# Kernel optimization log

Measured on AMD Instinct MI355X. Metric: run time of the kernel, lower is better.

The kernel has to match this reference:

```python
import jax, jax.numpy as jnp
import numpy as np

PERTURBATION_SCALE = 0.01

def setup_inputs() -> dict:
    key = jax.random.key(0)
    k1, k2, k3 = jax.random.split(key, 3)
    theta = jax.random.normal(k1, (256, 512), dtype=jnp.float32)
    basis_eval = jax.random.normal(k2, (100000, 512), dtype=jnp.float32)
    noise = jax.random.normal(k3, (256, 512), dtype=jnp.float32)
    return {"theta": theta, "basis_eval": basis_eval, "noise": noise}

def reference(theta, basis_eval, noise):
    # phi: [N, K] functional evaluations
    phi_raw = basis_eval @ theta.T
    phi_perturbed = basis_eval @ (theta + noise * PERTURBATION_SCALE).T
    # sign-crossings between consecutive evaluation points: [N-1, K]
    crossings = (phi_raw[:-1] * phi_raw[1:] < 0).astype(theta.dtype)
    crossings_p = (phi_perturbed[:-1] * phi_perturbed[1:] < 0).astype(theta.dtype)
    persistence = crossings * crossings_p  # [N-1, K]
    # fused pairwise shared-persistence: Gram matrix [K, K]
    gram = persistence.T @ persistence
    K = theta.shape[0]
    iu, ju = jnp.triu_indices(K, k=1)  # row-major i<j == itertools.combinations order
    return gram[iu, ju]  # [K*(K-1)/2]
```

## Files before the change

### kernel.cpp

```cpp
#include <hip/hip_runtime.h>
#include <hip/hip_bf16.h>
#include <stdint.h>

#define KDIM    256
#define NWORDS  1564
#define NW      1563
#define GEMM_GRID 1564

typedef float  f32x4  __attribute__((ext_vector_type(4)));
typedef __bf16 bf16x8 __attribute__((ext_vector_type(8)));

__device__ __forceinline__ void gl_lds16(const void* g, void* l) {
    __builtin_amdgcn_global_load_lds(
        (const __attribute__((address_space(1))) unsigned int*)g,
        (__attribute__((address_space(3))) unsigned int*)l, 16, 0, 0);
}

__global__ void build_w(const float* __restrict__ theta,
                        const float* __restrict__ noise,
                        __bf16* __restrict__ W) {
    int idx = blockIdx.x * 256 + threadIdx.x;
    int j = idx >> 9;
    int d = idx & 511;
    float v;
    if (j < KDIM) v = theta[j * 512 + d];
    else          v = theta[(j - KDIM) * 512 + d] + 0.01f * noise[(j - KDIM) * 512 + d];
    W[idx] = (__bf16)v;
}

__global__ void __launch_bounds__(512, 2)
gemm_signs(const float* __restrict__ basis,
           const __bf16* __restrict__ W,
           uint64_t* __restrict__ sbits) {
    __shared__ char smem[65536];

    const int tid    = threadIdx.x;
    const int lane   = tid & 63;
    const int wave   = tid >> 6;
    const int wr     = wave >> 2;
    const int wc     = wave & 3;
    const int lane16 = lane & 15;
    const int lgrp   = lane >> 4;

    const int orig = blockIdx.x;
    const int xcd  = orig & 7;
    const int wgid = (xcd < 4 ? xcd * 196 : 784 + (xcd - 4) * 195) + (orig >> 3);
    const int bn   = wgid & 1;
    const int bm   = wgid >> 1;

    auto stage = [&](int t) {
        char* abase = smem + ((t & 1) << 14);
        char* bbase = smem + 32768 + ((t & 1) << 14);
        #pragma unroll
        for (int i = 0; i < 2; ++i) {
            int r = wave * 16 + i * 8 + (lane >> 3);
            int g = lane & 7;
            int rg = bm * 128 + r; if (rg > 99999) rg = 99999;
            const float* src = basis + (size_t)rg * 512 + t * 32 + ((g ^ (r & 7)) << 2);
            gl_lds16(src, abase + (wave * 16 + i * 8) * 128);
        }
        #pragma unroll
        for (int i = 0; i < 2; ++i) {
            int c = wave * 32 + i * 16 + (lane >> 2);
            int g = lane & 3;
            const __bf16* src = W + (size_t)(bn * 256 + c) * 512 + t * 32
                                  + ((g ^ ((c >> 1) & 3)) << 3);
            gl_lds16(src, bbase + (wave * 32 + i * 16) * 64);
        }
    };

    stage(0);
    stage(1);

    f32x4 acc[4][4] = {};
    const int s = lane16 & 7;

    #pragma unroll
    for (int t = 0; t < 16; ++t) {
        if (t < 15) asm volatile("s_waitcnt vmcnt(4)\ns_barrier" ::: "memory");
        else        asm volatile("s_waitcnt vmcnt(0)\ns_barrier" ::: "memory");

        const char* ab = smem + ((t & 1) << 14);
        const char* bb = smem + 32768 + ((t & 1) << 14);

        bf16x8 bf[4];
        #pragma unroll
        for (int n = 0; n < 4; ++n) {
            int cc = wc * 64 + n * 16 + lane16;
            int gb = lgrp ^ ((cc >> 1) & 3);
            bf[n] = *(const bf16x8*)(bb + cc * 64 + gb * 16);
        }

        #pragma unroll
        for (int mh = 0; mh < 2; ++mh) {
            bf16x8 af[2];
            #pragma unroll
            for (int mi = 0; mi < 2; ++mi) {
                int rr = wr * 64 + (mh * 2 + mi) * 16 + lane16;
                f32x4 lo = *(const f32x4*)(ab + rr * 128 + (((2 * lgrp + 0) ^ s) << 4));
                f32x4 hi = *(const f32x4*)(ab + rr * 128 + (((2 * lgrp + 1) ^ s) << 4));
                af[mi][0] = (__bf16)lo[0]; af[mi][1] = (__bf16)lo[1];
                af[mi][2] = (__bf16)lo[2]; af[mi][3] = (__bf16)lo[3];
                af[mi][4] = (__bf16)hi[0]; af[mi][5] = (__bf16)hi[1];
                af[mi][6] = (__bf16)hi[2]; af[mi][7] = (__bf16)hi[3];
            }
            __builtin_amdgcn_s_setprio(1);
            #pragma unroll
            for (int mi = 0; mi < 2; ++mi)
                #pragma unroll
                for (int n = 0; n < 4; ++n)
                    acc[mh * 2 + mi][n] = __builtin_amdgcn_mfma_f32_16x16x32_bf16(
                        af[mi], bf[n], acc[mh * 2 + mi][n], 0, 0, 0);
            __builtin_amdgcn_s_setprio(0);
        }

        asm volatile("s_barrier" ::: "memory");
        if (t < 14) stage(t + 2);
    }

    unsigned char* sb = (unsigned char*)smem;
    #pragma unroll
    for (int m = 0; m < 4; ++m) {
        #pragma unroll
        for (int n = 0; n < 4; ++n) {
            int cc = wc * 64 + n * 16 + lane16;
            int rb = wr * 64 + m * 16 + lgrp * 4;
            uint32_t pk = 0;
            #pragma unroll
            for (int r = 0; r < 4; ++r)
                pk |= (acc[m][n][r] < 0.0f ? 1u : 0u) << (8 * r);
            *(uint32_t*)&sb[cc * 136 + rb] = pk;
        }
    }
    asm volatile("s_waitcnt lgkmcnt(0)\ns_barrier" ::: "memory");

    {
        const int col = tid & 255;
        const int wh  = tid >> 8;
        const unsigned char* src = &sb[col * 136 + wh * 64];
        uint64_t wbits = 0;
        #pragma unroll
        for (int k = 0; k < 16; ++k) {
            uint32_t q  = *(const uint32_t*)&src[4 * k];
            uint32_t p4 = ((q & 0x01010101u) * 0x10204080u) >> 28;
            wbits |= (uint64_t)p4 << (4 * k);
        }
        sbits[(size_t)(bm * 2 + wh) * 512 + bn * 256 + col] = wbits;
    }
}

__global__ void crossing_masks(const uint64_t* __restrict__ sbits,
                               uint64_t* __restrict__ maskT) {
    const int w = blockIdx.x;
    const int j = threadIdx.x;
    uint64_t s0r = sbits[(size_t)w * 512 + j];
    uint64_t s0p = sbits[(size_t)w * 512 + 256 + j];
    uint64_t s1r = sbits[(size_t)(w + 1) * 512 + j];
    uint64_t s1p = sbits[(size_t)(w + 1) * 512 + 256 + j];
    uint64_t cr = s0r ^ ((s0r >> 1) | (s1r << 63));
    uint64_t cp = s0p ^ ((s0p >> 1) | (s1p << 63));
    uint64_t m = cr & cp;
    if (w == NW - 1) m &= 0x7FFFFFFFull;
    maskT[(size_t)w * 256 + j] = m;
}

__global__ void zero_out(float* __restrict__ out) {
    int i = blockIdx.x * 256 + threadIdx.x;
    if (i < 32640) out[i] = 0.0f;
}

__global__ void pair_popcount(const uint64_t* __restrict__ maskT,
                              float* __restrict__ out) {
    const int i = blockIdx.x;
    const int c = blockIdx.y;
    const int j = threadIdx.x;
    if (j <= i) return;
    int w0 = c * 391;
    int w1 = w0 + 391; if (w1 > NW) w1 = NW;
    uint32_t sum = 0;
    #pragma unroll 4
    for (int w = w0; w < w1; ++w) {
        uint64_t mi = maskT[(size_t)w * 256 + i];
        uint64_t mj = maskT[(size_t)w * 256 + j];
        sum += (uint32_t)__popcll(mi & mj);
    }
    const size_t idx = (size_t)i * (2 * KDIM - i - 1) / 2 + (size_t)(j - i - 1);
    atomicAdd(&out[idx], (float)sum);
}

extern "C" void kernel_launch(void* const* d_in, const int* in_sizes, int n_in,
                              void* d_out, int out_size, void* d_ws, size_t ws_size,
                              hipStream_t stream) {
    const float* theta = (const float*)d_in[0];
    const float* basis = (const float*)d_in[1];
    const float* noise = (const float*)d_in[2];
    float* out = (float*)d_out;

    char* ws = (char*)d_ws;
    __bf16*   W     = (__bf16*)ws;
    uint64_t* sbits = (uint64_t*)(ws + 524288);
    uint64_t* maskT = (uint64_t*)(ws + 524288 + (size_t)NWORDS * 512 * 8);

    hipLaunchKernelGGL(build_w,        dim3(1024),     dim3(256), 0, stream, theta, noise, W);
    hipLaunchKernelGGL(gemm_signs,     dim3(GEMM_GRID),dim3(512), 0, stream, basis, W, sbits);
    hipLaunchKernelGGL(crossing_masks, dim3(NW),       dim3(256), 0, stream, sbits, maskT);
    hipLaunchKernelGGL(zero_out,       dim3(128),      dim3(256), 0, stream, out);
    hipLaunchKernelGGL(pair_popcount,  dim3(KDIM, 4),  dim3(256), 0, stream, maskT, out);
}
```

Baseline: 125.4 us.

## Stage A tile through registers as bf16 in LDS and raise GEMM occupancy

The GEMM kernel now loads the fp32 basis rows into registers, converts them to bf16 once, and stores them into a half-size LDS buffer. Previously fp32 went straight to LDS and was converted after every fragment read. This shrinks LDS to 48KB so launch bounds can request 4 blocks per SM, and it removes repeated conversion work from the MFMA loop. The A prefetch is register double-buffered with a different waitcnt schedule. Separately, pair_popcount is split into 8 chunks instead of 4 for more parallelism, at the cost of more atomics. Risks are register pressure from 4-block occupancy and extra VMEM latency exposure from the register path.

```diff
diff --git a/kernel.cpp b/kernel.cpp
--- a/kernel.cpp
+++ b/kernel.cpp
@@ -28,11 +28,11 @@
     W[idx] = (__bf16)v;
 }
 
-__global__ void __launch_bounds__(512, 2)
+__global__ void __launch_bounds__(512, 4)
 gemm_signs(const float* __restrict__ basis,
            const __bf16* __restrict__ W,
            uint64_t* __restrict__ sbits) {
-    __shared__ char smem[65536];
+    __shared__ char smem[49152];
 
     const int tid    = threadIdx.x;
     const int lane   = tid & 63;
@@ -48,17 +48,14 @@
     const int bn   = wgid & 1;
     const int bm   = wgid >> 1;
 
-    auto stage = [&](int t) {
-        char* abase = smem + ((t & 1) << 14);
-        char* bbase = smem + 32768 + ((t & 1) << 14);
-        #pragma unroll
-        for (int i = 0; i < 2; ++i) {
-            int r = wave * 16 + i * 8 + (lane >> 3);
-            int g = lane & 7;
-            int rg = bm * 128 + r; if (rg > 99999) rg = 99999;
-            const float* src = basis + (size_t)rg * 512 + t * 32 + ((g ^ (r & 7)) << 2);
-            gl_lds16(src, abase + (wave * 16 + i * 8) * 128);
-        }
+    const int ar = tid >> 2;
+    const int ah = tid & 3;
+    int arg = bm * 128 + ar; if (arg > 99999) arg = 99999;
+    const float* abase_g = basis + (size_t)arg * 512 + ah * 8;
+    const int awofs = ar * 64 + ((ah ^ (ar & 3)) << 4);
+
+    auto stage_B = [&](int t) {
+        char* bbase = smem + 16384 + ((t & 1) << 14);
         #pragma unroll
         for (int i = 0; i < 2; ++i) {
             int c = wave * 32 + i * 16 + (lane >> 2);
@@ -69,19 +66,38 @@
         }
     };
 
-    stage(0);
-    stage(1);
-
-    f32x4 acc[4][4] = {};
-    const int s = lane16 & 7;
+    f32x4  acc[4][4] = {};
+    float4 ra[2][2];
+
+    ra[0][0] = *(const float4*)(abase_g);
+    ra[0][1] = *(const float4*)(abase_g + 4);
+    ra[1][0] = *(const float4*)(abase_g + 32);
+    ra[1][1] = *(const float4*)(abase_g + 36);
+    stage_B(0);
+    asm volatile("s_waitcnt vmcnt(4)" ::: "memory");
+    {
+        bf16x8 a8;
+        a8[0] = (__bf16)ra[0][0].x; a8[1] = (__bf16)ra[0][0].y;
+        a8[2] = (__bf16)ra[0][0].z; a8[3] = (__bf16)ra[0][0].w;
+        a8[4] = (__bf16)ra[0][1].x; a8[5] = (__bf16)ra[0][1].y;
+        a8[6] = (__bf16)ra[0][1].z; a8[7] = (__bf16)ra[0][1].w;
+        *(bf16x8*)(smem + awofs) = a8;
+    }
 
     #pragma unroll
     for (int t = 0; t < 16; ++t) {
-        if (t < 15) asm volatile("s_waitcnt vmcnt(4)\ns_barrier" ::: "memory");
-        else        asm volatile("s_waitcnt vmcnt(0)\ns_barrier" ::: "memory");
-
-        const char* ab = smem + ((t & 1) << 14);
-        const char* bb = smem + 32768 + ((t & 1) << 14);
+        if (t < 14) {
+            ra[t & 1][0] = *(const float4*)(abase_g + (t + 2) * 32);
+            ra[t & 1][1] = *(const float4*)(abase_g + (t + 2) * 32 + 4);
+        }
+        if (t < 15) stage_B(t + 1);
+
+        if      (t < 14) asm volatile("s_waitcnt vmcnt(4)\ns_barrier" ::: "memory");
+        else if (t == 14) asm volatile("s_waitcnt vmcnt(2)\ns_barrier" ::: "memory");
+        else              asm volatile("s_waitcnt vmcnt(0)\ns_barrier" ::: "memory");
+
+        const char* ab = smem + ((t & 1) << 13);
+        const char* bb = smem + 16384 + ((t & 1) << 14);
 
         bf16x8 bf[4];
         #pragma unroll
@@ -90,32 +106,32 @@
             int gb = lgrp ^ ((cc >> 1) & 3);
             bf[n] = *(const bf16x8*)(bb + cc * 64 + gb * 16);
         }
-
-        #pragma unroll
-        for (int mh = 0; mh < 2; ++mh) {
-            bf16x8 af[2];
+        bf16x8 af[4];
+        #pragma unroll
+        for (int m = 0; m < 4; ++m) {
+            int rr = wr * 64 + m * 16 + lane16;
+            af[m] = *(const bf16x8*)(ab + rr * 64 + ((lgrp ^ (rr & 3)) << 4));
+        }
+
+        __builtin_amdgcn_s_setprio(1);
+        #pragma unroll
+        for (int m = 0; m < 4; ++m)
             #pragma unroll
-            for (int mi = 0; mi < 2; ++mi) {
-                int rr = wr * 64 + (mh * 2 + mi) * 16 + lane16;
-                f32x4 lo = *(const f32x4*)(ab + rr * 128 + (((2 * lgrp + 0) ^ s) << 4));
-                f32x4 hi = *(const f32x4*)(ab + rr * 128 + (((2 * lgrp + 1) ^ s) << 4));
-                af[mi][0] = (__bf16)lo[0]; af[mi][1] = (__bf16)lo[1];
-                af[mi][2] = (__bf16)lo[2]; af[mi][3] = (__bf16)lo[3];
-                af[mi][4] = (__bf16)hi[0]; af[mi][5] = (__bf16)hi[1];
-                af[mi][6] = (__bf16)hi[2]; af[mi][7] = (__bf16)hi[3];
-            }
-            __builtin_amdgcn_s_setprio(1);
-            #pragma unroll
-            for (int mi = 0; mi < 2; ++mi)
-                #pragma unroll
-                for (int n = 0; n < 4; ++n)
-                    acc[mh * 2 + mi][n] = __builtin_amdgcn_mfma_f32_16x16x32_bf16(
-                        af[mi], bf[n], acc[mh * 2 + mi][n], 0, 0, 0);
-            __builtin_amdgcn_s_setprio(0);
-        }
-
-        asm volatile("s_barrier" ::: "memory");
-        if (t < 14) stage(t + 2);
+            for (int n = 0; n < 4; ++n)
+                acc[m][n] = __builtin_amdgcn_mfma_f32_16x16x32_bf16(
+                    af[m], bf[n], acc[m][n], 0, 0, 0);
+        __builtin_amdgcn_s_setprio(0);
+
+        if (t < 15) {
+            bf16x8 a8;
+            a8[0] = (__bf16)ra[(t + 1) & 1][0].x; a8[1] = (__bf16)ra[(t + 1) & 1][0].y;
+            a8[2] = (__bf16)ra[(t + 1) & 1][0].z; a8[3] = (__bf16)ra[(t + 1) & 1][0].w;
+            a8[4] = (__bf16)ra[(t + 1) & 1][1].x; a8[5] = (__bf16)ra[(t + 1) & 1][1].y;
+            a8[6] = (__bf16)ra[(t + 1) & 1][1].z; a8[7] = (__bf16)ra[(t + 1) & 1][1].w;
+            *(bf16x8*)(smem + (((t + 1) & 1) << 13) + awofs) = a8;
+        }
+
+        asm volatile("s_waitcnt lgkmcnt(0)\ns_barrier" ::: "memory");
     }
 
     unsigned char* sb = (unsigned char*)smem;
@@ -175,8 +191,8 @@
     const int c = blockIdx.y;
     const int j = threadIdx.x;
     if (j <= i) return;
-    int w0 = c * 391;
-    int w1 = w0 + 391; if (w1 > NW) w1 = NW;
+    int w0 = c * 196;
+    int w1 = w0 + 196; if (w1 > NW) w1 = NW;
     uint32_t sum = 0;
     #pragma unroll 4
     for (int w = w0; w < w1; ++w) {
@@ -205,5 +221,5 @@
     hipLaunchKernelGGL(gemm_signs,     dim3(GEMM_GRID),dim3(512), 0, stream, basis, W, sbits);
     hipLaunchKernelGGL(crossing_masks, dim3(NW),       dim3(256), 0, stream, sbits, maskT);
     hipLaunchKernelGGL(zero_out,       dim3(128),      dim3(256), 0, stream, out);
-    hipLaunchKernelGGL(pair_popcount,  dim3(KDIM, 4),  dim3(256), 0, stream, maskT, out);
-}
+    hipLaunchKernelGGL(pair_popcount,  dim3(KDIM, 8),  dim3(256), 0, stream, maskT, out);
+}
```

New measurement: 127.9 us. +2.0%, slower.

## Convert A tile to bf16 in registers before LDS, use deeper K-steps, split popcount more

Applied to the files above, without the earlier changes.

The GEMM now loads the fp32 basis tile through registers, converts it to bf16 once and writes bf16 into LDS. Previously fp32 went straight to LDS and every wave converted it again on each read. K-step tiles double to 64 with fewer loop iterations, and MFMA groups are interleaved with LDS reads and the next A conversion. LDS use grows to 96KB, which may cut occupancy to one block per CU. The pair_popcount reduction is split into 8 chunks instead of 4 for more parallelism, at the cost of more atomics.

```diff
diff --git a/kernel.cpp b/kernel.cpp
--- a/kernel.cpp
+++ b/kernel.cpp
@@ -32,7 +32,7 @@
 gemm_signs(const float* __restrict__ basis,
            const __bf16* __restrict__ W,
            uint64_t* __restrict__ sbits) {
-    __shared__ char smem[65536];
+    __shared__ char smem[98304];
 
     const int tid    = threadIdx.x;
     const int lane   = tid & 63;
@@ -48,74 +48,143 @@
     const int bn   = wgid & 1;
     const int bm   = wgid >> 1;
 
-    auto stage = [&](int t) {
-        char* abase = smem + ((t & 1) << 14);
-        char* bbase = smem + 32768 + ((t & 1) << 14);
-        #pragma unroll
-        for (int i = 0; i < 2; ++i) {
-            int r = wave * 16 + i * 8 + (lane >> 3);
+    const int ar  = tid >> 2;
+    const int ah0 = (tid & 3) * 2;
+    int arg = bm * 128 + ar; if (arg > 99999) arg = 99999;
+    const float* ag0 = basis + (size_t)arg * 512 + ah0 * 8;
+    const float* ag1 = ag0 + 8;
+    const int aw0 = ar * 128 + (((ah0    ) ^ (ar & 7)) << 4);
+    const int aw1 = ar * 128 + (((ah0 + 1) ^ (ar & 7)) << 4);
+
+    auto stage_B = [&](int t) {
+        char* bbase = smem + 32768 + ((t & 1) << 15);
+        #pragma unroll
+        for (int i = 0; i < 4; ++i) {
+            int c = wave * 32 + i * 8 + (lane >> 3);
             int g = lane & 7;
-            int rg = bm * 128 + r; if (rg > 99999) rg = 99999;
-            const float* src = basis + (size_t)rg * 512 + t * 32 + ((g ^ (r & 7)) << 2);
-            gl_lds16(src, abase + (wave * 16 + i * 8) * 128);
-        }
-        #pragma unroll
-        for (int i = 0; i < 2; ++i) {
-            int c = wave * 32 + i * 16 + (lane >> 2);
-            int g = lane & 3;
-            const __bf16* src = W + (size_t)(bn * 256 + c) * 512 + t * 32
-                                  + ((g ^ ((c >> 1) & 3)) << 3);
-            gl_lds16(src, bbase + (wave * 32 + i * 16) * 64);
+            const __bf16* src = W + (size_t)(bn * 256 + c) * 512 + t * 64
+                                  + ((g ^ (c & 7)) << 3);
+            gl_lds16(src, bbase + (wave * 32 + i * 8) * 128);
         }
     };
 
-    stage(0);
-    stage(1);
-
-    f32x4 acc[4][4] = {};
-    const int s = lane16 & 7;
+    f32x4  acc[4][4] = {};
+    float4 ra[2][2];
+
+    auto cvt_write_A = [&](int q) {
+        char* abase = smem + (q << 14);
+        #pragma unroll
+        for (int u = 0; u < 2; ++u) {
+            bf16x8 a8;
+            a8[0] = (__bf16)ra[u][0].x; a8[1] = (__bf16)ra[u][0].y;
+            a8[2] = (__bf16)ra[u][0].z; a8[3] = (__bf16)ra[u][0].w;
+            a8[4] = (__bf16)ra[u][1].x; a8[5] = (__bf16)ra[u][1].y;
+            a8[6] = (__bf16)ra[u][1].z; a8[7] = (__bf16)ra[u][1].w;
+            *(bf16x8*)(abase + (u ? aw1 : aw0)) = a8;
+        }
+    };
+
+    ra[0][0] = *(const float4*)(ag0);  ra[0][1] = *(const float4*)(ag0 + 4);
+    ra[1][0] = *(const float4*)(ag1);  ra[1][1] = *(const float4*)(ag1 + 4);
+    stage_B(0);
+    asm volatile("s_waitcnt vmcnt(4)" ::: "memory");
+    cvt_write_A(0);
 
     #pragma unroll
-    for (int t = 0; t < 16; ++t) {
-        if (t < 15) asm volatile("s_waitcnt vmcnt(4)\ns_barrier" ::: "memory");
-        else        asm volatile("s_waitcnt vmcnt(0)\ns_barrier" ::: "memory");
-
-        const char* ab = smem + ((t & 1) << 14);
-        const char* bb = smem + 32768 + ((t & 1) << 14);
-
-        bf16x8 bf[4];
+    for (int t = 0; t < 8; ++t) {
+        const int p = t & 1, q = (t + 1) & 1;
+        const char* ab = smem + (p << 14);
+        const char* bb = smem + 32768 + (p << 15);
+
+        if (t < 7) {
+            ra[0][0] = *(const float4*)(ag0 + (t + 1) * 64);
+            ra[0][1] = *(const float4*)(ag0 + (t + 1) * 64 + 4);
+            ra[1][0] = *(const float4*)(ag1 + (t + 1) * 64);
+            ra[1][1] = *(const float4*)(ag1 + (t + 1) * 64 + 4);
+            stage_B(t + 1);
+            asm volatile("s_waitcnt vmcnt(8) lgkmcnt(0)\ns_barrier" ::: "memory");
+        } else {
+            asm volatile("s_waitcnt vmcnt(0) lgkmcnt(0)\ns_barrier" ::: "memory");
+        }
+
+        bf16x8 bf[4], af[2];
         #pragma unroll
         for (int n = 0; n < 4; ++n) {
             int cc = wc * 64 + n * 16 + lane16;
-            int gb = lgrp ^ ((cc >> 1) & 3);
-            bf[n] = *(const bf16x8*)(bb + cc * 64 + gb * 16);
-        }
-
-        #pragma unroll
-        for (int mh = 0; mh < 2; ++mh) {
-            bf16x8 af[2];
-            #pragma unroll
-            for (int mi = 0; mi < 2; ++mi) {
-                int rr = wr * 64 + (mh * 2 + mi) * 16 + lane16;
-                f32x4 lo = *(const f32x4*)(ab + rr * 128 + (((2 * lgrp + 0) ^ s) << 4));
-                f32x4 hi = *(const f32x4*)(ab + rr * 128 + (((2 * lgrp + 1) ^ s) << 4));
-                af[mi][0] = (__bf16)lo[0]; af[mi][1] = (__bf16)lo[1];
-                af[mi][2] = (__bf16)lo[2]; af[mi][3] = (__bf16)lo[3];
-                af[mi][4] = (__bf16)hi[0]; af[mi][5] = (__bf16)hi[1];
-                af[mi][6] = (__bf16)hi[2]; af[mi][7] = (__bf16)hi[3];
-            }
-            __builtin_amdgcn_s_setprio(1);
-            #pragma unroll
-            for (int mi = 0; mi < 2; ++mi)
-                #pragma unroll
-                for (int n = 0; n < 4; ++n)
-                    acc[mh * 2 + mi][n] = __builtin_amdgcn_mfma_f32_16x16x32_bf16(
-                        af[mi], bf[n], acc[mh * 2 + mi][n], 0, 0, 0);
-            __builtin_amdgcn_s_setprio(0);
-        }
-
-        asm volatile("s_barrier" ::: "memory");
-        if (t < 14) stage(t + 2);
+            bf[n] = *(const bf16x8*)(bb + cc * 128 + (((0 + lgrp) ^ (cc & 7)) << 4));
+        }
+        #pragma unroll
+        for (int mi = 0; mi < 2; ++mi) {
+            int rr = wr * 64 + mi * 16 + lane16;
+            af[mi] = *(const bf16x8*)(ab + rr * 128 + (((0 + lgrp) ^ (rr & 7)) << 4));
+        }
+        asm volatile("s_waitcnt lgkmcnt(0)" ::: "memory");
+        __builtin_amdgcn_sched_barrier(0);
+        __builtin_amdgcn_s_setprio(1);
+        #pragma unroll
+        for (int mi = 0; mi < 2; ++mi)
+            #pragma unroll
+            for (int n = 0; n < 4; ++n)
+                acc[mi][n] = __builtin_amdgcn_mfma_f32_16x16x32_bf16(af[mi], bf[n], acc[mi][n], 0, 0, 0);
+        __builtin_amdgcn_s_setprio(0);
+        asm volatile("s_barrier" ::: "memory");
+
+        #pragma unroll
+        for (int mi = 0; mi < 2; ++mi) {
+            int rr = wr * 64 + (2 + mi) * 16 + lane16;
+            af[mi] = *(const bf16x8*)(ab + rr * 128 + (((0 + lgrp) ^ (rr & 7)) << 4));
+        }
+        asm volatile("s_waitcnt lgkmcnt(0)" ::: "memory");
+        __builtin_amdgcn_sched_barrier(0);
+        __builtin_amdgcn_s_setprio(1);
+        #pragma unroll
+        for (int mi = 0; mi < 2; ++mi)
+            #pragma unroll
+            for (int n = 0; n < 4; ++n)
+                acc[2 + mi][n] = __builtin_amdgcn_mfma_f32_16x16x32_bf16(af[mi], bf[n], acc[2 + mi][n], 0, 0, 0);
+        __builtin_amdgcn_s_setprio(0);
+        asm volatile("s_barrier" ::: "memory");
+
+        #pragma unroll
+        for (int n = 0; n < 4; ++n) {
+            int cc = wc * 64 + n * 16 + lane16;
+            bf[n] = *(const bf16x8*)(bb + cc * 128 + (((4 + lgrp) ^ (cc & 7)) << 4));
+        }
+        #pragma unroll
+        for (int mi = 0; mi < 2; ++mi) {
+            int rr = wr * 64 + mi * 16 + lane16;
+            af[mi] = *(const bf16x8*)(ab + rr * 128 + (((4 + lgrp) ^ (rr & 7)) << 4));
+        }
+        asm volatile("s_waitcnt lgkmcnt(0)" ::: "memory");
+        __builtin_amdgcn_sched_barrier(0);
+        __builtin_amdgcn_s_setprio(1);
+        #pragma unroll
+        for (int mi = 0; mi < 2; ++mi)
+            #pragma unroll
+            for (int n = 0; n < 4; ++n)
+                acc[mi][n] = __builtin_amdgcn_mfma_f32_16x16x32_bf16(af[mi], bf[n], acc[mi][n], 0, 0, 0);
+        __builtin_amdgcn_s_setprio(0);
+        asm volatile("s_barrier" ::: "memory");
+
+        #pragma unroll
+        for (int mi = 0; mi < 2; ++mi) {
+            int rr = wr * 64 + (2 + mi) * 16 + lane16;
+            af[mi] = *(const bf16x8*)(ab + rr * 128 + (((4 + lgrp) ^ (rr & 7)) << 4));
+        }
+        if (t < 7) {
+            asm volatile("s_waitcnt vmcnt(4)" ::: "memory");
+            cvt_write_A(q);
+        }
+        asm volatile("s_waitcnt lgkmcnt(0)" ::: "memory");
+        __builtin_amdgcn_sched_barrier(0);
+        __builtin_amdgcn_s_setprio(1);
+        #pragma unroll
+        for (int mi = 0; mi < 2; ++mi)
+            #pragma unroll
+            for (int n = 0; n < 4; ++n)
+                acc[2 + mi][n] = __builtin_amdgcn_mfma_f32_16x16x32_bf16(af[mi], bf[n], acc[2 + mi][n], 0, 0, 0);
+        __builtin_amdgcn_s_setprio(0);
+        asm volatile("s_barrier" ::: "memory");
     }
 
     unsigned char* sb = (unsigned char*)smem;
@@ -141,8 +210,8 @@
         uint64_t wbits = 0;
         #pragma unroll
         for (int k = 0; k < 16; ++k) {
-            uint32_t q  = *(const uint32_t*)&src[4 * k];
-            uint32_t p4 = ((q & 0x01010101u) * 0x10204080u) >> 28;
+            uint32_t qv = *(const uint32_t*)&src[4 * k];
+            uint32_t p4 = ((qv & 0x01010101u) * 0x10204080u) >> 28;
             wbits |= (uint64_t)p4 << (4 * k);
         }
         sbits[(size_t)(bm * 2 + wh) * 512 + bn * 256 + col] = wbits;
@@ -175,8 +244,8 @@
     const int c = blockIdx.y;
     const int j = threadIdx.x;
     if (j <= i) return;
-    int w0 = c * 391;
-    int w1 = w0 + 391; if (w1 > NW) w1 = NW;
+    int w0 = c * 196;
+    int w1 = w0 + 196; if (w1 > NW) w1 = NW;
     uint32_t sum = 0;
     #pragma unroll 4
     for (int w = w0; w < w1; ++w) {
@@ -205,5 +274,5 @@
     hipLaunchKernelGGL(gemm_signs,     dim3(GEMM_GRID),dim3(512), 0, stream, basis, W, sbits);
     hipLaunchKernelGGL(crossing_masks, dim3(NW),       dim3(256), 0, stream, sbits, maskT);
     hipLaunchKernelGGL(zero_out,       dim3(128),      dim3(256), 0, stream, out);
-    hipLaunchKernelGGL(pair_popcount,  dim3(KDIM, 4),  dim3(256), 0, stream, maskT, out);
-}
+    hipLaunchKernelGGL(pair_popcount,  dim3(KDIM, 8),  dim3(256), 0, stream, maskT, out);
+}
```

After: 166.5 us. +32.8%, slower.
